# Kernel optimization log

Hardware: AMD Instinct MI355X
Metric: run time of the kernel (lower is better)

Reference implementation:

```python
import jax, jax.numpy as jnp
import numpy as np

L_PAIRS = 2
K_NEG = 64
TEMP = 0.1
EPS = 1e-8  # torch F.cosine_similarity default eps


def _cos(a, b):
    # cosine similarity along last axis, torch-style eps clamping of norms
    na = jnp.maximum(jnp.linalg.norm(a, axis=-1), EPS)
    nb = jnp.maximum(jnp.linalg.norm(b, axis=-1), EPS)
    return jnp.sum(a * b, axis=-1) / (na * nb)


def setup_inputs() -> dict:
    D, N, d = 64, 4096, 512
    key = jax.random.key(0)
    k0, k1, k2, k3 = jax.random.split(key, 4)
    return {
        "I_embeddings": jax.random.normal(k0, (D, N, d), dtype=jnp.float32),
        "g0": jax.random.normal(k1, (d,), dtype=jnp.float32),
        "g1": jax.random.normal(k2, (d,), dtype=jnp.float32),
        "g2": jax.random.normal(k3, (d,), dtype=jnp.float32),
    }


def reference(I_embeddings, g0, g1, g2):
    D, N, d = I_embeddings.shape
    T = TEMP

    # per-embedding full sum: [D, d]
    sums = jnp.sum(I_embeddings, axis=1)

    # hard-negative sums: drop the top-K rows by L2 norm per embedding
    norms = jnp.linalg.norm(I_embeddings, axis=2)              # [D, N]
    _, topk_idx = jax.lax.top_k(norms, K_NEG)                  # [D, K]
    keep = jnp.ones((D, N), dtype=bool)
    keep = keep.at[jnp.arange(D)[:, None], topk_idx].set(False)
    sums_neg = jnp.sum(I_embeddings * keep[:, :, None], axis=1)  # [D, d]

    samples = jnp.concatenate([sums, sums_neg], axis=0)        # [2D, d]

    # positive pairs (i, i+L)
    P = D - L_PAIRS
    i_idx = jnp.arange(P)
    j_idx = i_idx + L_PAIRS

    # candidates per pair: arange(2D) with i and j removed (i < j)
    base = jnp.arange(2 * D - 2)                               # [2D-2]
    cand = base[None, :] + (base[None, :] >= i_idx[:, None]).astype(base.dtype)
    cand = cand + (cand >= j_idx[:, None]).astype(cand.dtype)  # [P, 2D-2]

    # random choice of K_NEG negatives per pair (deterministic key)
    key = jax.random.key(42)
    keys = jax.random.split(key, P)
    perm = jax.vmap(lambda k: jax.random.permutation(k, 2 * D - 2))(keys)[:, :K_NEG]
    sel = jnp.take_along_axis(cand, perm, axis=1)              # [P, K]
    negs = samples[sel]                                        # [P, K, d]

    pos_ij = _cos(g1, jax.lax.stop_gradient(g2)) / T           # scalar
    pos_ji = _cos(g2, jax.lax.stop_gradient(g1)) / T           # scalar

    s_i = sums[i_idx]                                          # [P, d]
    s_j = sums[j_idx]
    sim_i = _cos(s_i[:, None, :], negs) / T                    # [P, K]
    sim_j = _cos(s_j[:, None, :], negs) / T

    # -log( exp(pos) / (exp(pos) + sum exp(sim)) ) = logaddexp(pos, lse(sim)) - pos
    loss_i = jnp.logaddexp(pos_ij, jax.nn.logsumexp(sim_i, axis=1)) - pos_ij  # [P]
    loss_j = jnp.logaddexp(pos_ji, jax.nn.logsumexp(sim_j, axis=1)) - pos_ji

    return jnp.sum(loss_i + loss_j)
```

## Files before the change

kernel.cpp:

```cpp
#include <hip/hip_runtime.h>
#include <stdint.h>

#define D_EMB   64
#define N_ROWS  4096
#define DIM     512
#define KNEG    64
#define P_PAIRS 62
#define BPE     32
#define RPB     (N_ROWS / BPE)
#define NCHUNK  (D_EMB * BPE)
#define EPSN    1e-8f
#define INV_T   10.0f
#define NEGINF  (-1e30f)

__device__ __forceinline__ uint32_t rotl32(uint32_t v, uint32_t r) {
  return (v << r) | (v >> (32u - r));
}

__device__ __forceinline__ void threefry(uint32_t k0, uint32_t k1,
                                         uint32_t c0, uint32_t c1,
                                         uint32_t& o0, uint32_t& o1) {
  uint32_t ks0 = k0, ks1 = k1, ks2 = k0 ^ k1 ^ 0x1BD11BDAu;
  uint32_t x0 = c0 + ks0, x1 = c1 + ks1;
#define RG(a,b,c,d) \
  x0 += x1; x1 = rotl32(x1,a); x1 ^= x0; \
  x0 += x1; x1 = rotl32(x1,b); x1 ^= x0; \
  x0 += x1; x1 = rotl32(x1,c); x1 ^= x0; \
  x0 += x1; x1 = rotl32(x1,d); x1 ^= x0;
  RG(13,15,26,6)   x0 += ks1; x1 += ks2 + 1u;
  RG(17,29,16,24)  x0 += ks2; x1 += ks0 + 2u;
  RG(13,15,26,6)   x0 += ks0; x1 += ks1 + 3u;
  RG(17,29,16,24)  x0 += ks1; x1 += ks2 + 4u;
  RG(13,15,26,6)   x0 += ks2; x1 += ks0 + 5u;
#undef RG
  o0 = x0; o1 = x1;
}

__global__ __launch_bounds__(256, 8) void k_pass1(const float* __restrict__ I,
                                                  float* __restrict__ partial,
                                                  float* __restrict__ norms) {
  const int e = blockIdx.x >> 5, b = blockIdx.x & 31;
  const int t = threadIdx.x, lane = t & 63, w = t >> 6;
  const float4* base = reinterpret_cast<const float4*>(I) + (size_t)e * N_ROWS * (DIM / 4);
  float acc[8] = {0.f,0.f,0.f,0.f,0.f,0.f,0.f,0.f};
  __shared__ float lds[4 * DIM];
  __shared__ float nlds[RPB];
  const int nbase = b * RPB;
  for (int i = 0; i < RPB / 4; ++i) {
    const int n = nbase + i * 4 + w;
    const float4* row = base + (size_t)n * (DIM / 4);
    float4 A = row[lane];
    float4 B = row[lane + 64];
    acc[0] += A.x; acc[1] += A.y; acc[2] += A.z; acc[3] += A.w;
    acc[4] += B.x; acc[5] += B.y; acc[6] += B.z; acc[7] += B.w;
    float sq = A.x*A.x + A.y*A.y + A.z*A.z + A.w*A.w
             + B.x*B.x + B.y*B.y + B.z*B.z + B.w*B.w;
#pragma unroll
    for (int off = 32; off; off >>= 1) sq += __shfl_xor(sq, off);
    if (lane == 0) nlds[i * 4 + w] = sqrtf(sq);
  }
  const int p0 = 4 * lane;
#pragma unroll
  for (int q = 0; q < 4; ++q) {
    lds[w * DIM + p0 + q]       = acc[q];
    lds[w * DIM + 256 + p0 + q] = acc[4 + q];
  }
  __syncthreads();
  float s0 = lds[t] + lds[DIM + t] + lds[2*DIM + t] + lds[3*DIM + t];
  float s1 = lds[256 + t] + lds[DIM + 256 + t] + lds[2*DIM + 256 + t] + lds[3*DIM + 256 + t];
  float* po = partial + (size_t)blockIdx.x * DIM;
  po[t] = s0;
  po[256 + t] = s1;
  if (t < RPB) norms[e * N_ROWS + nbase + t] = nlds[t];
}

#define CE(i, j) \
  { bool sw = (v##i < v##j) || (v##i == v##j && d##i > d##j);          \
    float tv = sw ? v##j : v##i; float uv = sw ? v##i : v##j;          \
    int   td = sw ? d##j : d##i; int   ud = sw ? d##i : d##j;          \
    v##i = tv; v##j = uv; d##i = td; d##j = ud; }

__global__ __launch_bounds__(512) void k_embed(const float* __restrict__ I,
                                               const float* __restrict__ partial,
                                               const float* __restrict__ norms,
                                               const float* __restrict__ g1,
                                               const float* __restrict__ g2,
                                               float* __restrict__ samples,
                                               float* __restrict__ snorm,
                                               float* __restrict__ posp,
                                               int* __restrict__ cnt2) {
  const int e = blockIdx.x;
  const int t = threadIdx.x, lane = t & 63, w = t >> 6;
  __shared__ float rA[8], rB[8], rC[8];

  if (e == D_EMB) {
    if (t == 0) cnt2[0] = 0;
    float x = g1[t], y = g2[t];
    float d = x * y, sa = x * x, sb = y * y;
#pragma unroll
    for (int off = 32; off; off >>= 1) {
      d  += __shfl_xor(d, off);
      sa += __shfl_xor(sa, off);
      sb += __shfl_xor(sb, off);
    }
    if (lane == 0) { rA[w] = d; rB[w] = sa; rC[w] = sb; }
    __syncthreads();
    if (t == 0) {
      float dt = 0.f, s1 = 0.f, s2 = 0.f;
      for (int q = 0; q < 8; ++q) { dt += rA[q]; s1 += rB[q]; s2 += rC[q]; }
      posp[0] = dt / (fmaxf(sqrtf(s1), EPSN) * fmaxf(sqrtf(s2), EPSN)) * INV_T;
    }
    return;
  }

  __shared__ float cval[8 * KNEG];
  __shared__ int   cidx[8 * KNEG];
  __shared__ int   topidx[KNEG];

  float v0 = norms[e*N_ROWS + 0*512 + t], v1 = norms[e*N_ROWS + 1*512 + t];
  float v2 = norms[e*N_ROWS + 2*512 + t], v3 = norms[e*N_ROWS + 3*512 + t];
  float v4 = norms[e*N_ROWS + 4*512 + t], v5 = norms[e*N_ROWS + 5*512 + t];
  float v6 = norms[e*N_ROWS + 6*512 + t], v7 = norms[e*N_ROWS + 7*512 + t];
  int d0 = 0*512+t, d1 = 1*512+t, d2 = 2*512+t, d3 = 3*512+t;
  int d4 = 4*512+t, d5 = 5*512+t, d6 = 6*512+t, d7 = 7*512+t;
  CE(0,1) CE(2,3) CE(4,5) CE(6,7)
  CE(0,2) CE(1,3) CE(4,6) CE(5,7)
  CE(1,2) CE(5,6)
  CE(0,4) CE(1,5) CE(2,6) CE(3,7)
  CE(2,4) CE(3,5)
  CE(1,2) CE(3,4) CE(5,6)

  for (int k = 0; k < KNEG; ++k) {
    float bv = v0; int bi = d0;
#pragma unroll
    for (int off = 32; off; off >>= 1) {
      float ov = __shfl_xor(bv, off);
      int   oi = __shfl_xor(bi, off);
      if (ov > bv || (ov == bv && oi < bi)) { bv = ov; bi = oi; }
    }
    if (lane == 0) { cval[w * KNEG + k] = bv; cidx[w * KNEG + k] = bi; }
    if (v0 == bv && d0 == bi) {
      v0=v1; d0=d1; v1=v2; d1=d2; v2=v3; d2=d3; v3=v4; d3=d4;
      v4=v5; d4=d5; v5=v6; d5=d6; v6=v7; d6=d7; v7=NEGINF; d7=0x7fffffff;
    }
  }
  __syncthreads();

  if (w == 0) {
    int p = 0;
    float hv = (lane < 8) ? cval[lane * KNEG] : NEGINF;
    int   hi = (lane < 8) ? cidx[lane * KNEG] : 0x7fffffff;
    for (int k = 0; k < KNEG; ++k) {
      float bv = hv; int bi = hi;
#pragma unroll
      for (int off = 4; off; off >>= 1) {
        float ov = __shfl_xor(bv, off, 8);
        int   oi = __shfl_xor(bi, off, 8);
        if (ov > bv || (ov == bv && oi < bi)) { bv = ov; bi = oi; }
      }
      if (lane == 0) topidx[k] = bi;
      if (lane < 8 && hv == bv && hi == bi) {
        ++p;
        hv = (p < KNEG) ? cval[lane * KNEG + p] : NEGINF;
        hi = (p < KNEG) ? cidx[lane * KNEG + p] : 0x7fffffff;
      }
    }
  }
  __syncthreads();

  float s = 0.f;
  for (int b2 = 0; b2 < BPE; ++b2)
    s += partial[(size_t)(e * BPE + b2) * DIM + t];

  const float* base = I + (size_t)e * N_ROWS * DIM;
  float a = 0.f;
#pragma unroll 4
  for (int k = 0; k < KNEG; ++k)
    a += base[(size_t)topidx[k] * DIM + t];
  float sn = s - a;

  float q1 = s * s, q2 = sn * sn;
#pragma unroll
  for (int off = 32; off; off >>= 1) {
    q1 += __shfl_xor(q1, off);
    q2 += __shfl_xor(q2, off);
  }
  if (lane == 0) { rA[w] = q1; rB[w] = q2; }
  __syncthreads();
  if (t == 0) {
    float n1 = 0.f, n2 = 0.f;
    for (int q = 0; q < 8; ++q) { n1 += rA[q]; n2 += rB[q]; }
    snorm[e]         = fmaxf(sqrtf(n1), EPSN);
    snorm[D_EMB + e] = fmaxf(sqrtf(n2), EPSN);
  }
  samples[(size_t)e * DIM + t]           = s;
  samples[(size_t)(D_EMB + e) * DIM + t] = sn;
}

__global__ __launch_bounds__(256) void k_p3p4(const float* __restrict__ samples,
                                              const float* __restrict__ snorm,
                                              const float* __restrict__ posp,
                                              float* __restrict__ pairloss,
                                              int* __restrict__ cnt2,
                                              float* __restrict__ out) {
  const int p = blockIdx.x;
  const int t = threadIdx.x, lane = t & 63, w = t >> 6;
  __shared__ uint32_t bits[126];
  __shared__ uint32_t sk[2];
  __shared__ int      sel[KNEG];
  __shared__ float    simi[KNEG], simj[KNEG];
  __shared__ int      flag;

  if (t == 0) {
    uint32_t kh, kl, a, b;
    threefry(0u, 42u, 0u, (uint32_t)p, kh, kl);
    threefry(kh, kl, 0u, 1u, a, b);
    sk[0] = a; sk[1] = b;
  }
  __syncthreads();
  if (t < 126) {
    uint32_t a, b;
    threefry(sk[0], sk[1], 0u, (uint32_t)t, a, b);
    bits[t] = a ^ b;
  }
  __syncthreads();
  if (t < 126) {
    const uint32_t myb = bits[t];
    int rank = 0;
    for (int j = 0; j < 126; ++j) {
      const uint32_t bj = bits[j];
      rank += ((bj < myb) || (bj == myb && j < t)) ? 1 : 0;
    }
    if (rank < KNEG) {
      int vv = t + (t >= p ? 1 : 0);
      vv += (vv >= p + 2 ? 1 : 0);
      sel[rank] = vv;
    }
  }
  __syncthreads();

  const float4* S = reinterpret_cast<const float4*>(samples);
  const float4 siA = S[p * 128 + lane],       siB = S[p * 128 + 64 + lane];
  const float4 sjA = S[(p + 2) * 128 + lane], sjB = S[(p + 2) * 128 + 64 + lane];
  const float ni = snorm[p], nj = snorm[p + 2];
  for (int k = w; k < KNEG; k += 4) {
    const int r = sel[k];
    const float4 vA = S[r * 128 + lane], vB = S[r * 128 + 64 + lane];
    float di = siA.x*vA.x + siA.y*vA.y + siA.z*vA.z + siA.w*vA.w
             + siB.x*vB.x + siB.y*vB.y + siB.z*vB.z + siB.w*vB.w;
    float dj = sjA.x*vA.x + sjA.y*vA.y + sjA.z*vA.z + sjA.w*vA.w
             + sjB.x*vB.x + sjB.y*vB.y + sjB.z*vB.z + sjB.w*vB.w;
#pragma unroll
    for (int off = 32; off; off >>= 1) {
      di += __shfl_xor(di, off);
      dj += __shfl_xor(dj, off);
    }
    if (lane == 0) {
      const float nr = snorm[r];
      simi[k] = di / (ni * nr) * INV_T;
      simj[k] = dj / (nj * nr) * INV_T;
    }
  }
  __syncthreads();
  if (t < KNEG) {
    const float xi = simi[t], xj = simj[t];
    float mi = xi, mj = xj;
#pragma unroll
    for (int off = 32; off; off >>= 1) {
      mi = fmaxf(mi, __shfl_xor(mi, off));
      mj = fmaxf(mj, __shfl_xor(mj, off));
    }
    float ei = expf(xi - mi), ej = expf(xj - mj);
#pragma unroll
    for (int off = 32; off; off >>= 1) {
      ei += __shfl_xor(ei, off);
      ej += __shfl_xor(ej, off);
    }
    if (t == 0) {
      const float pos = posp[0];
      const float lsei = mi + logf(ei), lsej = mj + logf(ej);
      const float li = fmaxf(pos, lsei) + log1pf(expf(-fabsf(pos - lsei))) - pos;
      const float lj = fmaxf(pos, lsej) + log1pf(expf(-fabsf(pos - lsej))) - pos;
      pairloss[p] = li + lj;
    }
  }
  __syncthreads();

  if (t == 0) {
    int old = __hip_atomic_fetch_add(cnt2, 1, __ATOMIC_ACQ_REL,
                                     __HIP_MEMORY_SCOPE_AGENT);
    flag = (old == P_PAIRS - 1) ? 1 : 0;
  }
  __syncthreads();
  const int trig = flag;
  __syncthreads();
  if (!trig) return;
  __builtin_amdgcn_fence(__ATOMIC_ACQUIRE, "agent");
  if (t < 64) {
    float vv = (t < P_PAIRS) ? pairloss[t] : 0.f;
#pragma unroll
    for (int off = 32; off; off >>= 1) vv += __shfl_xor(vv, off);
    if (t == 0) out[0] = vv;
  }
}

extern "C" void kernel_launch(void* const* d_in, const int* in_sizes, int n_in,
                              void* d_out, int out_size, void* d_ws, size_t ws_size,
                              hipStream_t stream) {
  const float* I  = (const float*)d_in[0];
  const float* g1 = (const float*)d_in[2];
  const float* g2 = (const float*)d_in[3];
  float* out = (float*)d_out;

  float* ws = (float*)d_ws;
  float* norms    = ws;
  float* partial  = ws + 262144;
  float* samples  = partial + 1048576;
  float* snorm    = samples + 65536;
  float* posp     = snorm + 128;
  float* pairloss = posp + 4;
  int*   cnt2     = (int*)(pairloss + 64);

  k_pass1<<<NCHUNK,    256, 0, stream>>>(I, partial, norms);
  k_embed<<<D_EMB + 1, 512, 0, stream>>>(I, partial, norms, g1, g2,
                                         samples, snorm, posp, cnt2);
  k_p3p4 <<<P_PAIRS,   256, 0, stream>>>(samples, snorm, posp, pairloss,
                                         cnt2, out);
}
```

Before: 190.4 us.

## Unroll pass1 row loads eight-deep and halve blocks per embedding

The first pass now issues eight row loads per warp per iteration, which raises memory-level parallelism for the 512MB streaming read. Each warp handles a contiguous 64-row slab instead of interleaved rows. Blocks per embedding drop from 32 to 16, so there are fewer partial sums to reduce later, and the occupancy hint changes from 8 to 4. The cost is higher register pressure and fewer blocks to hide latency.

```diff
diff --git a/kernel.cpp b/kernel.cpp
--- a/kernel.cpp
+++ b/kernel.cpp
@@ -6,7 +6,7 @@
 #define DIM     512
 #define KNEG    64
 #define P_PAIRS 62
-#define BPE     32
+#define BPE     16
 #define RPB     (N_ROWS / BPE)
 #define NCHUNK  (D_EMB * BPE)
 #define EPSN    1e-8f
@@ -36,29 +36,59 @@
   o0 = x0; o1 = x1;
 }
 
-__global__ __launch_bounds__(256, 8) void k_pass1(const float* __restrict__ I,
+__global__ __launch_bounds__(256, 4) void k_pass1(const float* __restrict__ I,
                                                   float* __restrict__ partial,
                                                   float* __restrict__ norms) {
-  const int e = blockIdx.x >> 5, b = blockIdx.x & 31;
+  const int e = blockIdx.x >> 4, b = blockIdx.x & 15;
   const int t = threadIdx.x, lane = t & 63, w = t >> 6;
-  const float4* base = reinterpret_cast<const float4*>(I) + (size_t)e * N_ROWS * (DIM / 4);
-  float acc[8] = {0.f,0.f,0.f,0.f,0.f,0.f,0.f,0.f};
+  const float4* base4 = reinterpret_cast<const float4*>(I) + (size_t)e * N_ROWS * (DIM / 4);
+  const int nbase = b * RPB;
+  const int wrow = w * (RPB / 4);
   __shared__ float lds[4 * DIM];
   __shared__ float nlds[RPB];
-  const int nbase = b * RPB;
-  for (int i = 0; i < RPB / 4; ++i) {
-    const int n = nbase + i * 4 + w;
-    const float4* row = base + (size_t)n * (DIM / 4);
-    float4 A = row[lane];
-    float4 B = row[lane + 64];
-    acc[0] += A.x; acc[1] += A.y; acc[2] += A.z; acc[3] += A.w;
-    acc[4] += B.x; acc[5] += B.y; acc[6] += B.z; acc[7] += B.w;
-    float sq = A.x*A.x + A.y*A.y + A.z*A.z + A.w*A.w
-             + B.x*B.x + B.y*B.y + B.z*B.z + B.w*B.w;
-#pragma unroll
-    for (int off = 32; off; off >>= 1) sq += __shfl_xor(sq, off);
-    if (lane == 0) nlds[i * 4 + w] = sqrtf(sq);
-  }
+  float acc[8] = {0.f,0.f,0.f,0.f,0.f,0.f,0.f,0.f};
+
+  for (int i = 0; i < 8; ++i) {
+    const int lr = wrow + i * 8;
+    const int idx = (nbase + lr) * (DIM / 4) + lane;
+    float4 A0 = base4[idx + 0*128], B0 = base4[idx + 0*128 + 64];
+    float4 A1 = base4[idx + 1*128], B1 = base4[idx + 1*128 + 64];
+    float4 A2 = base4[idx + 2*128], B2 = base4[idx + 2*128 + 64];
+    float4 A3 = base4[idx + 3*128], B3 = base4[idx + 3*128 + 64];
+    float4 A4 = base4[idx + 4*128], B4 = base4[idx + 4*128 + 64];
+    float4 A5 = base4[idx + 5*128], B5 = base4[idx + 5*128 + 64];
+    float4 A6 = base4[idx + 6*128], B6 = base4[idx + 6*128 + 64];
+    float4 A7 = base4[idx + 7*128], B7 = base4[idx + 7*128 + 64];
+
+    acc[0] += A0.x + A1.x + A2.x + A3.x + A4.x + A5.x + A6.x + A7.x;
+    acc[1] += A0.y + A1.y + A2.y + A3.y + A4.y + A5.y + A6.y + A7.y;
+    acc[2] += A0.z + A1.z + A2.z + A3.z + A4.z + A5.z + A6.z + A7.z;
+    acc[3] += A0.w + A1.w + A2.w + A3.w + A4.w + A5.w + A6.w + A7.w;
+    acc[4] += B0.x + B1.x + B2.x + B3.x + B4.x + B5.x + B6.x + B7.x;
+    acc[5] += B0.y + B1.y + B2.y + B3.y + B4.y + B5.y + B6.y + B7.y;
+    acc[6] += B0.z + B1.z + B2.z + B3.z + B4.z + B5.z + B6.z + B7.z;
+    acc[7] += B0.w + B1.w + B2.w + B3.w + B4.w + B5.w + B6.w + B7.w;
+
+#define SQ(r) (A##r.x*A##r.x + A##r.y*A##r.y + A##r.z*A##r.z + A##r.w*A##r.w \
+             + B##r.x*B##r.x + B##r.y*B##r.y + B##r.z*B##r.z + B##r.w*B##r.w)
+    float s0 = SQ(0), s1 = SQ(1), s2 = SQ(2), s3 = SQ(3);
+    float s4 = SQ(4), s5 = SQ(5), s6 = SQ(6), s7 = SQ(7);
+#undef SQ
+#pragma unroll
+    for (int off = 32; off; off >>= 1) {
+      s0 += __shfl_xor(s0, off); s1 += __shfl_xor(s1, off);
+      s2 += __shfl_xor(s2, off); s3 += __shfl_xor(s3, off);
+      s4 += __shfl_xor(s4, off); s5 += __shfl_xor(s5, off);
+      s6 += __shfl_xor(s6, off); s7 += __shfl_xor(s7, off);
+    }
+    if (lane == 0) {
+      nlds[lr]     = sqrtf(s0); nlds[lr + 1] = sqrtf(s1);
+      nlds[lr + 2] = sqrtf(s2); nlds[lr + 3] = sqrtf(s3);
+      nlds[lr + 4] = sqrtf(s4); nlds[lr + 5] = sqrtf(s5);
+      nlds[lr + 6] = sqrtf(s6); nlds[lr + 7] = sqrtf(s7);
+    }
+  }
+
   const int p0 = 4 * lane;
 #pragma unroll
   for (int q = 0; q < 4; ++q) {
@@ -71,7 +101,7 @@
   float* po = partial + (size_t)blockIdx.x * DIM;
   po[t] = s0;
   po[256 + t] = s1;
-  if (t < RPB) norms[e * N_ROWS + nbase + t] = nlds[t];
+  norms[e * N_ROWS + nbase + t] = nlds[t];
 }
 
 #define CE(i, j) \
@@ -315,7 +345,7 @@
   float* ws = (float*)d_ws;
   float* norms    = ws;
   float* partial  = ws + 262144;
-  float* samples  = partial + 1048576;
+  float* samples  = partial + 524288;
   float* snorm    = samples + 65536;
   float* posp     = snorm + 128;
   float* pairloss = posp + 4;
```

New measurement: 193.3 us. No clear change (+1.5%).
